# Kernel optimization log

Measured on AMD Instinct MI355X. Metric: run time of the kernel, lower is better.

The kernel has to match this reference:

```python
import jax, jax.numpy as jnp
import numpy as np

N_NODES = 100000


def gcn_conv(x, edge_index, W, b):
    # PyG GCNConv: h = D^{-1/2} (A + I) D^{-1/2} (x @ W) + b
    N = x.shape[0]
    h = x @ W  # [N, C_out]
    loops = jnp.arange(N, dtype=edge_index.dtype)
    src = jnp.concatenate([edge_index[0], loops])
    dst = jnp.concatenate([edge_index[1], loops])
    deg = jax.ops.segment_sum(jnp.ones_like(dst, dtype=h.dtype), dst, num_segments=N)
    inv_sqrt = jnp.where(deg > 0, jax.lax.rsqrt(deg), 0.0)
    norm = inv_sqrt[src] * inv_sqrt[dst]              # [E+N]
    msg = h[src] * norm[:, None]                      # gather + scale
    out = jax.ops.segment_sum(msg, dst, num_segments=N)  # scatter-add
    return out + b


def setup_inputs() -> dict:
    key = jax.random.key(0)
    ks = jax.random.split(key, 6)
    x = jax.random.normal(ks[0], (N_NODES, 4), dtype=jnp.float32)
    edge_index = jax.random.randint(ks[1], (2, 3200000), 0, N_NODES, dtype=jnp.int32)
    edge_label_index = jax.random.randint(ks[2], (2, 200000), 0, N_NODES, dtype=jnp.int32)
    W1 = jax.random.normal(ks[3], (4, 128), dtype=jnp.float32) * (1.0 / np.sqrt(4))
    b1 = jnp.zeros((128,), dtype=jnp.float32)
    W2 = jax.random.normal(ks[4], (128, 64), dtype=jnp.float32) * (1.0 / np.sqrt(128))
    b2 = jnp.zeros((64,), dtype=jnp.float32)
    return {"x": x, "edge_index": edge_index, "edge_label_index": edge_label_index,
            "W1": W1, "b1": b1, "W2": W2, "b2": b2}


def reference(x, edge_index, edge_label_index, W1, b1, W2, b2):
    h = jax.nn.relu(gcn_conv(x, edge_index, W1, b1))
    z = gcn_conv(h, edge_index, W2, b2)               # encode -> [N, 64]
    # decode: dot product per labeled edge -> [E_lbl]
    logits = jnp.sum(z[edge_label_index[0]] * z[edge_label_index[1]], axis=-1)
    return logits
```

## Files before the change

kernel.cpp:

```cpp
#include <hip/hip_runtime.h>

#define N_NODES 100000
#define N_EDGES 3200000
#define N_LBL   200000
#define C1 128
#define C2 64

#define BSH   7
#define NPB   128
#define NBKT  ((N_NODES + NPB - 1) / NPB)
#define NCB   500
#define PPT   512
#define CHUNK (N_EDGES / NCB)
#define CAP   4992

#define RSTRIDE 132

__device__ __forceinline__ float4 f4add(float4 a, float4 b) {
    return make_float4(a.x + b.x, a.y + b.y, a.z + b.z, a.w + b.w);
}
__device__ __forceinline__ unsigned short f2bf(float f) {
    unsigned int u = __float_as_uint(f);
    u += 0x7fff + ((u >> 16) & 1);
    return (unsigned short)(u >> 16);
}
__device__ __forceinline__ float bflo(unsigned int u) {
    return __uint_as_float(u << 16);
}
__device__ __forceinline__ float bfhi(unsigned int u) {
    return __uint_as_float(u & 0xffff0000u);
}

__global__ __launch_bounds__(PPT) void pair_place_kernel(const int* __restrict__ ei,
        int* __restrict__ gcursor, unsigned int* __restrict__ pairs) {
    __shared__ int hist[NBKT];
    __shared__ int cur[NBKT];
    int tid = threadIdx.x;
    for (int i = tid; i < NBKT; i += PPT) hist[i] = 0;
    __syncthreads();
    int base = blockIdx.x * CHUNK;
    unsigned int pk[13]; int bkt[13]; int rnk[13];
    #pragma unroll
    for (int k = 0; k < 13; ++k) {
        if (k < 12 || tid < CHUNK - 12 * PPT) {
            int e = base + k * PPT + tid;
            int s = ei[e], d = ei[N_EDGES + e];
            int b = d >> BSH;
            bkt[k] = b;
            pk[k] = ((unsigned int)(d & (NPB - 1)) << 17) | (unsigned int)s;
            rnk[k] = atomicAdd(&hist[b], 1);
        }
    }
    __syncthreads();
    for (int i = tid; i < NBKT; i += PPT) {
        int h = hist[i];
        cur[i] = h ? (i * CAP + atomicAdd(&gcursor[i], h)) : 0;
    }
    __syncthreads();
    #pragma unroll
    for (int k = 0; k < 13; ++k) {
        if (k < 12 || tid < CHUNK - 12 * PPT) {
            int pos = cur[bkt[k]] + rnk[k];
            pos = min(pos, NBKT * CAP - 1);
            pairs[pos] = pk[k];
        }
    }
}

__global__ __launch_bounds__(512) void bucket_finish_kernel(
        const unsigned int* __restrict__ pairs, const int* __restrict__ gcursor,
        const float4* __restrict__ x, int* __restrict__ offs, int* __restrict__ ends,
        float* __restrict__ inv, float4* __restrict__ xs, int* __restrict__ srcs) {
    __shared__ int deg[NPB];
    __shared__ int nstart[NPB];
    __shared__ int wsum2[2];
    int tid = threadIdx.x;
    int b = blockIdx.x;
    int nbase = b << BSH;
    int eb = b * CAP;
    int ee = eb + min(gcursor[b], CAP);
    if (tid < NPB) deg[tid] = 0;
    __syncthreads();
    unsigned int pk[10]; int rnk[10];
    #pragma unroll
    for (int k = 0; k < 10; ++k) {
        int j = eb + k * 512 + tid;
        if (j < ee) {
            unsigned int p = pairs[j];
            pk[k] = p;
            rnk[k] = atomicAdd(&deg[p >> 17], 1);
        }
    }
    __syncthreads();
    int v = 0, incl = 0;
    if (tid < NPB) {
        int lane = tid & 63;
        v = deg[tid];
        incl = v;
        #pragma unroll
        for (int off = 1; off < 64; off <<= 1) {
            int t = __shfl_up(incl, off);
            if (lane >= off) incl += t;
        }
        if (lane == 63) wsum2[tid >> 6] = incl;
    }
    __syncthreads();
    if (tid < NPB) {
        int excl = incl - v + ((tid >= 64) ? wsum2[0] : 0);
        int start = eb + excl;
        nstart[tid] = start;
        int n = nbase + tid;
        if (n < N_NODES) {
            offs[n] = start;
            ends[n] = start + v;
            float iv = rsqrtf((float)(v + 1));
            inv[n] = iv;
            float4 xv = x[n];
            xv.x *= iv; xv.y *= iv; xv.z *= iv; xv.w *= iv;
            xs[n] = xv;
        }
    }
    __syncthreads();
    #pragma unroll
    for (int k = 0; k < 10; ++k) {
        int j = eb + k * 512 + tid;
        if (j < ee) {
            unsigned int p = pk[k];
            srcs[nstart[p >> 17] + rnk[k]] = (int)(p & 0x1FFFFu);
        }
    }
}

__global__ __launch_bounds__(256) void agg1_gemm12_kernel(
        const float4* __restrict__ xs, const int* __restrict__ offs,
        const int* __restrict__ ends, const int* __restrict__ srcs,
        const float* __restrict__ inv, const float* __restrict__ W1,
        const float* __restrict__ b1, const float* __restrict__ W2,
        unsigned short* __restrict__ hs2b) {
    __shared__ float w1s[4 * C1];
    __shared__ float bs[C1];
    __shared__ float w2s[C1 * C2];
    __shared__ float rows[64 * RSTRIDE];
    __shared__ float4 aggt[64];
    int tid = threadIdx.x;
    int base = blockIdx.x * 64;
    w1s[tid] = W1[tid];
    w1s[tid + 256] = W1[tid + 256];
    if (tid < C1) bs[tid] = b1[tid];
    {
        const float4* w4 = (const float4*)W2;
        float4* s4 = (float4*)w2s;
        for (int i = tid; i < C1 * C2 / 4; i += 256) s4[i] = w4[i];
    }
    int nd = tid >> 2, g = tid & 3;
    int n = base + nd;
    {
        float4 acc = make_float4(0.f, 0.f, 0.f, 0.f);
        if (n < N_NODES) {
            if (g == 0) acc = xs[n];
            int e = ends[n];
            for (int j = offs[n] + g; j < e; j += 4)
                acc = f4add(acc, xs[srcs[j]]);
        }
        acc.x += __shfl_xor(acc.x, 1); acc.y += __shfl_xor(acc.y, 1);
        acc.z += __shfl_xor(acc.z, 1); acc.w += __shfl_xor(acc.w, 1);
        acc.x += __shfl_xor(acc.x, 2); acc.y += __shfl_xor(acc.y, 2);
        acc.z += __shfl_xor(acc.z, 2); acc.w += __shfl_xor(acc.w, 2);
        if (g == 0) aggt[nd] = acc;
    }
    __syncthreads();
    {
        float s = (n < N_NODES) ? inv[n] : 0.f;
        float4 t = aggt[nd];
        t.x *= s; t.y *= s; t.z *= s; t.w *= s;
        #pragma unroll 8
        for (int cc = 0; cc < 32; ++cc) {
            int c = g + 4 * cc;
            float h = t.x * w1s[c] + t.y * w1s[C1 + c] + t.z * w1s[2 * C1 + c]
                    + t.w * w1s[3 * C1 + c] + bs[c];
            rows[nd * RSTRIDE + c] = fmaxf(h, 0.f);
        }
    }
    __syncthreads();
    int q = tid & 15;
    int ng = tid >> 4;
    float4 acc[4];
    #pragma unroll
    for (int j = 0; j < 4; ++j) acc[j] = make_float4(0.f, 0.f, 0.f, 0.f);
    #pragma unroll 4
    for (int k = 0; k < C1; ++k) {
        float4 wv = *(const float4*)(w2s + k * C2 + q * 4);
        #pragma unroll
        for (int j = 0; j < 4; ++j) {
            float r = rows[(ng * 4 + j) * RSTRIDE + k];
            acc[j].x += r * wv.x; acc[j].y += r * wv.y;
            acc[j].z += r * wv.z; acc[j].w += r * wv.w;
        }
    }
    #pragma unroll
    for (int j = 0; j < 4; ++j) {
        int m = base + ng * 4 + j;
        if (m < N_NODES) {
            float s = inv[m];
            ushort4 o;
            o.x = f2bf(acc[j].x * s); o.y = f2bf(acc[j].y * s);
            o.z = f2bf(acc[j].z * s); o.w = f2bf(acc[j].w * s);
            *((ushort4*)(hs2b + (size_t)m * C2) + q) = o;
        }
    }
}

__global__ void agg2_kernel(const unsigned short* __restrict__ hs2b,
                            const int* __restrict__ offs, const int* __restrict__ ends,
                            const int* __restrict__ srcs, const float* __restrict__ inv,
                            const float4* __restrict__ b2,
                            unsigned short* __restrict__ zb) {
    int gid = blockIdx.x * blockDim.x + threadIdx.x;
    int n = gid >> 6;
    if (n >= N_NODES) return;
    int lane = gid & 63;
    int q = lane & 7;
    int g = lane >> 3;
    float acc[8] = {0.f, 0.f, 0.f, 0.f, 0.f, 0.f, 0.f, 0.f};
    if (g == 0) {
        uint4 v = *((const uint4*)(hs2b + (size_t)n * C2) + q);
        acc[0] += bflo(v.x); acc[1] += bfhi(v.x);
        acc[2] += bflo(v.y); acc[3] += bfhi(v.y);
        acc[4] += bflo(v.z); acc[5] += bfhi(v.z);
        acc[6] += bflo(v.w); acc[7] += bfhi(v.w);
    }
    int e = ends[n];
    int j = offs[n] + g;
    for (; j + 24 < e; j += 32) {
        int s0 = srcs[j];
        int s1 = srcs[j + 8];
        int s2 = srcs[j + 16];
        int s3 = srcs[j + 24];
        uint4 v0 = *((const uint4*)(hs2b + (size_t)s0 * C2) + q);
        uint4 v1 = *((const uint4*)(hs2b + (size_t)s1 * C2) + q);
        uint4 v2 = *((const uint4*)(hs2b + (size_t)s2 * C2) + q);
        uint4 v3 = *((const uint4*)(hs2b + (size_t)s3 * C2) + q);
        acc[0] += bflo(v0.x); acc[1] += bfhi(v0.x);
        acc[2] += bflo(v0.y); acc[3] += bfhi(v0.y);
        acc[4] += bflo(v0.z); acc[5] += bfhi(v0.z);
        acc[6] += bflo(v0.w); acc[7] += bfhi(v0.w);
        acc[0] += bflo(v1.x); acc[1] += bfhi(v1.x);
        acc[2] += bflo(v1.y); acc[3] += bfhi(v1.y);
        acc[4] += bflo(v1.z); acc[5] += bfhi(v1.z);
        acc[6] += bflo(v1.w); acc[7] += bfhi(v1.w);
        acc[0] += bflo(v2.x); acc[1] += bfhi(v2.x);
        acc[2] += bflo(v2.y); acc[3] += bfhi(v2.y);
        acc[4] += bflo(v2.z); acc[5] += bfhi(v2.z);
        acc[6] += bflo(v2.w); acc[7] += bfhi(v2.w);
        acc[0] += bflo(v3.x); acc[1] += bfhi(v3.x);
        acc[2] += bflo(v3.y); acc[3] += bfhi(v3.y);
        acc[4] += bflo(v3.z); acc[5] += bfhi(v3.z);
        acc[6] += bflo(v3.w); acc[7] += bfhi(v3.w);
    }
    for (; j < e; j += 8) {
        int s0 = srcs[j];
        uint4 v0 = *((const uint4*)(hs2b + (size_t)s0 * C2) + q);
        acc[0] += bflo(v0.x); acc[1] += bfhi(v0.x);
        acc[2] += bflo(v0.y); acc[3] += bfhi(v0.y);
        acc[4] += bflo(v0.z); acc[5] += bfhi(v0.z);
        acc[6] += bflo(v0.w); acc[7] += bfhi(v0.w);
    }
    #pragma unroll
    for (int k = 0; k < 8; ++k) {
        acc[k] += __shfl_xor(acc[k], 8);
        acc[k] += __shfl_xor(acc[k], 16);
        acc[k] += __shfl_xor(acc[k], 32);
    }
    if (g == 0) {
        float s = inv[n];
        float4 b0 = b2[q * 2], b1v = b2[q * 2 + 1];
        float o0 = acc[0] * s + b0.x,  o1 = acc[1] * s + b0.y;
        float o2 = acc[2] * s + b0.z,  o3 = acc[3] * s + b0.w;
        float o4 = acc[4] * s + b1v.x, o5 = acc[5] * s + b1v.y;
        float o6 = acc[6] * s + b1v.z, o7 = acc[7] * s + b1v.w;
        uint4 w;
        w.x = (unsigned int)f2bf(o0) | ((unsigned int)f2bf(o1) << 16);
        w.y = (unsigned int)f2bf(o2) | ((unsigned int)f2bf(o3) << 16);
        w.z = (unsigned int)f2bf(o4) | ((unsigned int)f2bf(o5) << 16);
        w.w = (unsigned int)f2bf(o6) | ((unsigned int)f2bf(o7) << 16);
        ((uint4*)(zb + (size_t)n * C2))[q] = w;
    }
}

__global__ void decode_kernel(const int* __restrict__ eli,
                              const unsigned short* __restrict__ zb,
                              float* __restrict__ out) {
    int gid = blockIdx.x * blockDim.x + threadIdx.x;
    int e = gid >> 3;
    if (e >= N_LBL) return;
    int q = gid & 7;
    int a = eli[e], b = eli[N_LBL + e];
    uint4 va = ((const uint4*)zb)[(size_t)a * 8 + q];
    uint4 vb = ((const uint4*)zb)[(size_t)b * 8 + q];
    float p = bflo(va.x) * bflo(vb.x) + bfhi(va.x) * bfhi(vb.x)
            + bflo(va.y) * bflo(vb.y) + bfhi(va.y) * bfhi(vb.y)
            + bflo(va.z) * bflo(vb.z) + bfhi(va.z) * bfhi(vb.z)
            + bflo(va.w) * bflo(vb.w) + bfhi(va.w) * bfhi(vb.w);
    p += __shfl_xor(p, 4);
    p += __shfl_xor(p, 2);
    p += __shfl_xor(p, 1);
    if (q == 0) out[e] = p;
}

extern "C" void kernel_launch(void* const* d_in, const int* in_sizes, int n_in,
                              void* d_out, int out_size, void* d_ws, size_t ws_size,
                              hipStream_t stream) {
    const float* x  = (const float*)d_in[0];
    const int*   ei = (const int*)d_in[1];
    const int*  eli = (const int*)d_in[2];
    const float* W1 = (const float*)d_in[3];
    const float* b1 = (const float*)d_in[4];
    const float* W2 = (const float*)d_in[5];
    const float* b2 = (const float*)d_in[6];
    float* out = (float*)d_out;

    char* p = (char*)d_ws;
    int*   gcursor = (int*)p;   p += 1024 * 4;
    int*   offs    = (int*)p;   p += (size_t)N_NODES * 4;
    int*   ends    = (int*)p;   p += (size_t)N_NODES * 4;
    float* inv     = (float*)p; p += (size_t)N_NODES * 4;
    unsigned int* pairs = (unsigned int*)p; p += (size_t)NBKT * CAP * 4;
    int*   srcs    = (int*)p;   p += (size_t)NBKT * CAP * 4;
    float* xs      = (float*)p; p += (size_t)N_NODES * 16;
    unsigned short* hs2b = (unsigned short*)p; p += (size_t)N_NODES * C2 * 2;
    unsigned short* zb   = (unsigned short*)p; p += (size_t)N_NODES * C2 * 2;

    hipMemsetAsync(gcursor, 0, NBKT * 4, stream);
    pair_place_kernel<<<NCB, PPT, 0, stream>>>(ei, gcursor, pairs);
    bucket_finish_kernel<<<NBKT, 512, 0, stream>>>(pairs, gcursor, (const float4*)x,
                                                   offs, ends, inv, (float4*)xs, srcs);
    agg1_gemm12_kernel<<<(N_NODES + 63) / 64, 256, 0, stream>>>(
        (const float4*)xs, offs, ends, srcs, inv, W1, b1, W2, hs2b);
    agg2_kernel<<<((size_t)N_NODES * 64 + 255) / 256, 256, 0, stream>>>(
        hs2b, offs, ends, srcs, inv, (const float4*)b2, zb);
    decode_kernel<<<((size_t)N_LBL * 8 + 255) / 256, 256, 0, stream>>>(eli, zb, out);
}
```

Baseline: 258.2 us.

## Split layer-1 aggregation out of the fused GEMM kernel and shrink agg2 unroll

```diff
diff --git a/kernel.cpp b/kernel.cpp
--- a/kernel.cpp
+++ b/kernel.cpp
@@ -131,9 +131,25 @@
     }
 }
 
-__global__ __launch_bounds__(256) void agg1_gemm12_kernel(
-        const float4* __restrict__ xs, const int* __restrict__ offs,
-        const int* __restrict__ ends, const int* __restrict__ srcs,
+__global__ void agg1_kernel(const float4* __restrict__ xs, const int* __restrict__ offs,
+                            const int* __restrict__ ends, const int* __restrict__ srcs,
+                            float4* __restrict__ aggX) {
+    int gid = blockIdx.x * blockDim.x + threadIdx.x;
+    int n = gid >> 2;
+    if (n >= N_NODES) return;
+    int g = gid & 3;
+    float4 acc = (g == 0) ? xs[n] : make_float4(0.f, 0.f, 0.f, 0.f);
+    int e = ends[n];
+    for (int j = offs[n] + g; j < e; j += 4)
+        acc = f4add(acc, xs[srcs[j]]);
+    acc.x += __shfl_xor(acc.x, 1); acc.y += __shfl_xor(acc.y, 1);
+    acc.z += __shfl_xor(acc.z, 1); acc.w += __shfl_xor(acc.w, 1);
+    acc.x += __shfl_xor(acc.x, 2); acc.y += __shfl_xor(acc.y, 2);
+    acc.z += __shfl_xor(acc.z, 2); acc.w += __shfl_xor(acc.w, 2);
+    if (g == 0) aggX[n] = acc;
+}
+
+__global__ __launch_bounds__(256) void gemm12_kernel(const float4* __restrict__ aggX,
         const float* __restrict__ inv, const float* __restrict__ W1,
         const float* __restrict__ b1, const float* __restrict__ W2,
         unsigned short* __restrict__ hs2b) {
@@ -141,7 +157,6 @@
     __shared__ float bs[C1];
     __shared__ float w2s[C1 * C2];
     __shared__ float rows[64 * RSTRIDE];
-    __shared__ float4 aggt[64];
     int tid = threadIdx.x;
     int base = blockIdx.x * 64;
     w1s[tid] = W1[tid];
@@ -152,30 +167,17 @@
         float4* s4 = (float4*)w2s;
         for (int i = tid; i < C1 * C2 / 4; i += 256) s4[i] = w4[i];
     }
-    int nd = tid >> 2, g = tid & 3;
-    int n = base + nd;
+    __syncthreads();
     {
-        float4 acc = make_float4(0.f, 0.f, 0.f, 0.f);
-        if (n < N_NODES) {
-            if (g == 0) acc = xs[n];
-            int e = ends[n];
-            for (int j = offs[n] + g; j < e; j += 4)
-                acc = f4add(acc, xs[srcs[j]]);
-        }
-        acc.x += __shfl_xor(acc.x, 1); acc.y += __shfl_xor(acc.y, 1);
-        acc.z += __shfl_xor(acc.z, 1); acc.w += __shfl_xor(acc.w, 1);
-        acc.x += __shfl_xor(acc.x, 2); acc.y += __shfl_xor(acc.y, 2);
-        acc.z += __shfl_xor(acc.z, 2); acc.w += __shfl_xor(acc.w, 2);
-        if (g == 0) aggt[nd] = acc;
-    }
-    __syncthreads();
-    {
-        float s = (n < N_NODES) ? inv[n] : 0.f;
-        float4 t = aggt[nd];
+        int nd = tid >> 2, p = tid & 3;
+        int n = base + nd;
+        float4 t = make_float4(0.f, 0.f, 0.f, 0.f);
+        float s = 0.f;
+        if (n < N_NODES) { t = aggX[n]; s = inv[n]; }
         t.x *= s; t.y *= s; t.z *= s; t.w *= s;
         #pragma unroll 8
         for (int cc = 0; cc < 32; ++cc) {
-            int c = g + 4 * cc;
+            int c = p + 4 * cc;
             float h = t.x * w1s[c] + t.y * w1s[C1 + c] + t.z * w1s[2 * C1 + c]
                     + t.w * w1s[3 * C1 + c] + bs[c];
             rows[nd * RSTRIDE + c] = fmaxf(h, 0.f);
@@ -231,15 +233,11 @@
     }
     int e = ends[n];
     int j = offs[n] + g;
-    for (; j + 24 < e; j += 32) {
+    for (; j + 8 < e; j += 16) {
         int s0 = srcs[j];
         int s1 = srcs[j + 8];
-        int s2 = srcs[j + 16];
-        int s3 = srcs[j + 24];
         uint4 v0 = *((const uint4*)(hs2b + (size_t)s0 * C2) + q);
         uint4 v1 = *((const uint4*)(hs2b + (size_t)s1 * C2) + q);
-        uint4 v2 = *((const uint4*)(hs2b + (size_t)s2 * C2) + q);
-        uint4 v3 = *((const uint4*)(hs2b + (size_t)s3 * C2) + q);
         acc[0] += bflo(v0.x); acc[1] += bfhi(v0.x);
         acc[2] += bflo(v0.y); acc[3] += bfhi(v0.y);
         acc[4] += bflo(v0.z); acc[5] += bfhi(v0.z);
@@ -248,16 +246,8 @@
         acc[2] += bflo(v1.y); acc[3] += bfhi(v1.y);
         acc[4] += bflo(v1.z); acc[5] += bfhi(v1.z);
         acc[6] += bflo(v1.w); acc[7] += bfhi(v1.w);
-        acc[0] += bflo(v2.x); acc[1] += bfhi(v2.x);
-        acc[2] += bflo(v2.y); acc[3] += bfhi(v2.y);
-        acc[4] += bflo(v2.z); acc[5] += bfhi(v2.z);
-        acc[6] += bflo(v2.w); acc[7] += bfhi(v2.w);
-        acc[0] += bflo(v3.x); acc[1] += bfhi(v3.x);
-        acc[2] += bflo(v3.y); acc[3] += bfhi(v3.y);
-        acc[4] += bflo(v3.z); acc[5] += bfhi(v3.z);
-        acc[6] += bflo(v3.w); acc[7] += bfhi(v3.w);
-    }
-    for (; j < e; j += 8) {
+    }
+    if (j < e) {
         int s0 = srcs[j];
         uint4 v0 = *((const uint4*)(hs2b + (size_t)s0 * C2) + q);
         acc[0] += bflo(v0.x); acc[1] += bfhi(v0.x);
@@ -327,6 +317,7 @@
     unsigned int* pairs = (unsigned int*)p; p += (size_t)NBKT * CAP * 4;
     int*   srcs    = (int*)p;   p += (size_t)NBKT * CAP * 4;
     float* xs      = (float*)p; p += (size_t)N_NODES * 16;
+    float* aggX    = (float*)p; p += (size_t)N_NODES * 16;
     unsigned short* hs2b = (unsigned short*)p; p += (size_t)N_NODES * C2 * 2;
     unsigned short* zb   = (unsigned short*)p; p += (size_t)N_NODES * C2 * 2;
 
@@ -334,8 +325,10 @@
     pair_place_kernel<<<NCB, PPT, 0, stream>>>(ei, gcursor, pairs);
     bucket_finish_kernel<<<NBKT, 512, 0, stream>>>(pairs, gcursor, (const float4*)x,
                                                    offs, ends, inv, (float4*)xs, srcs);
-    agg1_gemm12_kernel<<<(N_NODES + 63) / 64, 256, 0, stream>>>(
-        (const float4*)xs, offs, ends, srcs, inv, W1, b1, W2, hs2b);
+    agg1_kernel<<<(N_NODES * 4 + 255) / 256, 256, 0, stream>>>((const float4*)xs, offs,
+                                                               ends, srcs, (float4*)aggX);
+    gemm12_kernel<<<(N_NODES + 63) / 64, 256, 0, stream>>>((const float4*)aggX, inv,
+                                                           W1, b1, W2, hs2b);
     agg2_kernel<<<((size_t)N_NODES * 64 + 255) / 256, 256, 0, stream>>>(
         hs2b, offs, ends, srcs, inv, (const float4*)b2, zb);
     decode_kernel<<<((size_t)N_LBL * 8 + 255) / 256, 256, 0, stream>>>(eli, zb, out);
```

New measurement: 261.6 us. No clear change (+1.3%).
